# Performance work log

Hardware: AMD Instinct MI355X
Metric: run time of the kernel (lower is better)

The kernel has to match this reference:

```python
import jax, jax.numpy as jnp
import numpy as np

IN_FEATURES = 2048
OUT_FEATURES = 2048
ORDER = 8
BATCH = 8192


def setup_inputs() -> dict:
    key = jax.random.key(0)
    k1, k2, k3, k4 = jax.random.split(key, 4)
    x = jax.random.normal(k1, (BATCH, IN_FEATURES), dtype=jnp.float32)
    v = jax.random.normal(k2, (ORDER, max(IN_FEATURES, OUT_FEATURES)), dtype=jnp.float32)
    d = jax.random.normal(k3, (min(IN_FEATURES, OUT_FEATURES),), dtype=jnp.float32)
    bias = jax.random.normal(k4, (OUT_FEATURES,), dtype=jnp.float32) * 0.01
    return {"x": x, "v": v, "d": d, "bias": bias}


def reference(x, v, d, bias):
    # Normalize each reflection vector (row-wise L2 norm), as in the torch module.
    n = v.shape[1]  # max_feature = 2048
    vn = v / jnp.linalg.norm(v, axis=1, keepdims=True)
    # Householder matrices H_i = I - 2 v_i v_i^T, shape [order, n, n]
    H = jnp.eye(n, dtype=x.dtype)[None, :, :] - 2.0 * jnp.einsum('ab,ac->abc', vn, vn)
    # Chain multiply u = H_0 @ H_1 @ ... @ H_{order-1} (order is a small static constant)
    u = H[0]
    for i in range(1, H.shape[0]):
        u = u @ H[i]
    # out_features <= in_features branch: W = u @ (eye(in, out) @ diag(d))
    # eye(in, out) @ diag(d) places d on the leading diagonal of an [in, out] matrix,
    # so W = u[:, :out] * d (column scaling) -- same math, no dense diag matmul.
    W = u[:, :OUT_FEATURES] * d[None, :]
    y = x @ W + bias[None, :]
    return y
```

## Files before the change

kernel.cpp:

```cpp
#include <hip/hip_runtime.h>

#define N_FEAT 2048
#define ORDER 8
#define BATCH 8192
#define BLOCK 256
#define ROWS 4
#define NPAIR 28
#define NVAL 32

typedef float v4f __attribute__((ext_vector_type(4)));

__device__ __forceinline__ float dot4(v4f a, v4f b) {
    return a.x * b.x + a.y * b.y + a.z * b.z + a.w * b.w;
}

__global__ __launch_bounds__(BLOCK) void prep_kernel(
    const float* __restrict__ v, float* __restrict__ vn,
    float* __restrict__ Tm) {
    const int tid = threadIdx.x;
    const int lane = tid & 63, wid = tid >> 6;

    v4f a0[ORDER], a1[ORDER];
    #pragma unroll
    for (int i = 0; i < ORDER; ++i) {
        a0[i] = *(const v4f*)(v + (size_t)i * N_FEAT + tid * 4);
        a1[i] = *(const v4f*)(v + (size_t)i * N_FEAT + 1024 + tid * 4);
    }
    float ss[ORDER];
    #pragma unroll
    for (int i = 0; i < ORDER; ++i)
        ss[i] = dot4(a0[i], a0[i]) + dot4(a1[i], a1[i]);
    #pragma unroll
    for (int o = 32; o > 0; o >>= 1)
        #pragma unroll
        for (int i = 0; i < ORDER; ++i) ss[i] += __shfl_down(ss[i], o, 64);

    __shared__ float red[4][ORDER];
    __shared__ float gred[4][NPAIR];
    if (lane == 0) {
        #pragma unroll
        for (int i = 0; i < ORDER; ++i) red[wid][i] = ss[i];
    }
    __syncthreads();
    #pragma unroll
    for (int i = 0; i < ORDER; ++i) {
        const float inv = 1.0f / sqrtf(red[0][i] + red[1][i] + red[2][i] + red[3][i]);
        a0[i] *= inv; a1[i] *= inv;
        *(v4f*)(vn + (size_t)i * N_FEAT + tid * 4) = a0[i];
        *(v4f*)(vn + (size_t)i * N_FEAT + 1024 + tid * 4) = a1[i];
    }

    float gp[NPAIR];
    {
        int idx = 0;
        #pragma unroll
        for (int j = 0; j < ORDER; ++j)
            #pragma unroll
            for (int k = j + 1; k < ORDER; ++k)
                gp[idx++] = dot4(a0[j], a0[k]) + dot4(a1[j], a1[k]);
    }
    #pragma unroll
    for (int o = 32; o > 0; o >>= 1)
        #pragma unroll
        for (int q = 0; q < NPAIR; ++q) gp[q] += __shfl_down(gp[q], o, 64);
    if (lane == 0) {
        #pragma unroll
        for (int q = 0; q < NPAIR; ++q) gred[wid][q] = gp[q];
    }
    __syncthreads();

    if (tid == 0) {
        float G[ORDER][ORDER];
        {
            int idx = 0;
            #pragma unroll
            for (int j = 0; j < ORDER; ++j)
                #pragma unroll
                for (int k = j + 1; k < ORDER; ++k) {
                    G[j][k] = gred[0][idx] + gred[1][idx] + gred[2][idx] + gred[3][idx];
                    ++idx;
                }
        }
        float T[ORDER][ORDER];
        #pragma unroll
        for (int j = 0; j < ORDER; ++j)
            #pragma unroll
            for (int k = 0; k < ORDER; ++k) T[j][k] = 0.0f;
        T[0][0] = 2.0f;
        #pragma unroll
        for (int k = 1; k < ORDER; ++k) {
            #pragma unroll
            for (int j = 0; j < k; ++j) {
                float s = 0.0f;
                #pragma unroll
                for (int m = j; m < k; ++m) s += T[j][m] * G[m][k];
                T[j][k] = -2.0f * s;
            }
            T[k][k] = 2.0f;
        }
        #pragma unroll
        for (int j = 0; j < ORDER; ++j)
            #pragma unroll
            for (int k = 0; k < ORDER; ++k)
                Tm[j * ORDER + k] = T[j][k];
    }
}

__global__ __launch_bounds__(BLOCK, 3) void orth_apply_kernel(
    const float* __restrict__ x, const float* __restrict__ vn,
    const float* __restrict__ Tm, const float* __restrict__ d,
    const float* __restrict__ bias, float* __restrict__ y) {
    const int tid = threadIdx.x;
    const int lane = tid & 63;
    const size_t base = (size_t)blockIdx.x * ROWS * N_FEAT;
    const int c0 = tid * 4;
    const int c1 = 1024 + tid * 4;

    __shared__ v4f S4[NVAL / 4];
    float* Sf = (float*)S4;
    if (tid < NVAL) Sf[tid] = 0.0f;
    __syncthreads();

    v4f a0[ORDER], a1[ORDER];
    #pragma unroll
    for (int i = 0; i < ORDER; ++i) {
        a0[i] = *(const v4f*)(vn + (size_t)i * N_FEAT + c0);
        a1[i] = *(const v4f*)(vn + (size_t)i * N_FEAT + c1);
    }

    v4f z0[ROWS], z1[ROWS];
    #pragma unroll
    for (int r = 0; r < ROWS; ++r) {
        z0[r] = __builtin_nontemporal_load((const v4f*)(x + base + (size_t)r * N_FEAT + c0));
        z1[r] = __builtin_nontemporal_load((const v4f*)(x + base + (size_t)r * N_FEAT + c1));
    }

    float s[NVAL];
    #pragma unroll
    for (int i = 0; i < ORDER; ++i)
        #pragma unroll
        for (int r = 0; r < ROWS; ++r)
            s[r * ORDER + i] = dot4(z0[r], a0[i]) + dot4(z1[r], a1[i]);

    #pragma unroll
    for (int step = 0; step < 5; ++step) {
        const int m = 1 << step;
        const int n = NVAL >> step;
        #pragma unroll
        for (int j = 0; j < n / 2; ++j) {
            const float a = s[2 * j], b = s[2 * j + 1];
            const float keep = (lane & m) ? b : a;
            const float send = (lane & m) ? a : b;
            s[j] = keep + __shfl_xor(send, m, 64);
        }
    }

    atomicAdd(&Sf[lane & (NVAL - 1)], s[0]);
    __syncthreads();

    v4f Sv[NVAL / 4];
    #pragma unroll
    for (int k = 0; k < NVAL / 4; ++k) Sv[k] = S4[k];
    #define PVAL(r, j) (Sv[((r) * ORDER + (j)) >> 2][((r) * ORDER + (j)) & 3])

    float c[ROWS][ORDER];
    #pragma unroll
    for (int i = 0; i < ORDER; ++i)
        #pragma unroll
        for (int r = 0; r < ROWS; ++r) {
            float acc = 0.0f;
            #pragma unroll
            for (int j = 0; j <= i; ++j)
                acc += PVAL(r, j) * Tm[j * ORDER + i];
            c[r][i] = acc;
        }

    #pragma unroll
    for (int i = 0; i < ORDER; ++i)
        #pragma unroll
        for (int r = 0; r < ROWS; ++r) {
            z0[r] -= c[r][i] * a0[i];
            z1[r] -= c[r][i] * a1[i];
        }

    const v4f d0 = *(const v4f*)(d + c0);
    const v4f d1 = *(const v4f*)(d + c1);
    const v4f b0 = *(const v4f*)(bias + c0);
    const v4f b1 = *(const v4f*)(bias + c1);
    #pragma unroll
    for (int r = 0; r < ROWS; ++r) {
        v4f o0 = z0[r] * d0 + b0;
        v4f o1 = z1[r] * d1 + b1;
        __builtin_nontemporal_store(o0, (v4f*)(y + base + (size_t)r * N_FEAT + c0));
        __builtin_nontemporal_store(o1, (v4f*)(y + base + (size_t)r * N_FEAT + c1));
    }
}

extern "C" void kernel_launch(void* const* d_in, const int* in_sizes, int n_in,
                              void* d_out, int out_size, void* d_ws, size_t ws_size,
                              hipStream_t stream) {
    const float* x    = (const float*)d_in[0];
    const float* v    = (const float*)d_in[1];
    const float* d    = (const float*)d_in[2];
    const float* bias = (const float*)d_in[3];
    float* y  = (float*)d_out;
    float* vn = (float*)d_ws;
    float* Tm = vn + ORDER * N_FEAT;

    prep_kernel<<<1, BLOCK, 0, stream>>>(v, vn, Tm);
    orth_apply_kernel<<<BATCH / ROWS, BLOCK, 0, stream>>>(x, vn, Tm, d, bias, y);
}
```

Measured before the change: 136.8 us.

## Split fused orthogonal apply into projection and finish kernels

Splits the fused kernel into a projection kernel that writes per-row Householder coefficients to a workspace buffer and a finish kernel that rereads x and applies the correction, bias and scaling. This removes the block-wide reduction barrier from the pass that holds x in registers and allows higher occupancy in the finish pass. The cost is a second full read of x plus an extra launch. A fallback keeps the fused kernel when the workspace is too small.

```diff
diff --git a/kernel.cpp b/kernel.cpp
--- a/kernel.cpp
+++ b/kernel.cpp
@@ -103,6 +103,114 @@
             #pragma unroll
             for (int k = 0; k < ORDER; ++k)
                 Tm[j * ORDER + k] = T[j][k];
+    }
+}
+
+__global__ __launch_bounds__(BLOCK, 3) void proj_kernel(
+    const float* __restrict__ x, const float* __restrict__ vn,
+    const float* __restrict__ Tm, float* __restrict__ cbuf) {
+    const int tid = threadIdx.x;
+    const int lane = tid & 63;
+    const size_t base = (size_t)blockIdx.x * ROWS * N_FEAT;
+    const int c0 = tid * 4;
+    const int c1 = 1024 + tid * 4;
+
+    __shared__ float Sf[NVAL];
+    if (tid < NVAL) Sf[tid] = 0.0f;
+    __syncthreads();
+
+    v4f a0[ORDER], a1[ORDER];
+    #pragma unroll
+    for (int i = 0; i < ORDER; ++i) {
+        a0[i] = *(const v4f*)(vn + (size_t)i * N_FEAT + c0);
+        a1[i] = *(const v4f*)(vn + (size_t)i * N_FEAT + c1);
+    }
+    v4f z0[ROWS], z1[ROWS];
+    #pragma unroll
+    for (int r = 0; r < ROWS; ++r) {
+        z0[r] = *(const v4f*)(x + base + (size_t)r * N_FEAT + c0);
+        z1[r] = *(const v4f*)(x + base + (size_t)r * N_FEAT + c1);
+    }
+
+    float s[NVAL];
+    #pragma unroll
+    for (int i = 0; i < ORDER; ++i)
+        #pragma unroll
+        for (int r = 0; r < ROWS; ++r)
+            s[r * ORDER + i] = dot4(z0[r], a0[i]) + dot4(z1[r], a1[i]);
+
+    #pragma unroll
+    for (int step = 0; step < 5; ++step) {
+        const int m = 1 << step;
+        const int n = NVAL >> step;
+        #pragma unroll
+        for (int j = 0; j < n / 2; ++j) {
+            const float a = s[2 * j], b = s[2 * j + 1];
+            const float keep = (lane & m) ? b : a;
+            const float send = (lane & m) ? a : b;
+            s[j] = keep + __shfl_xor(send, m, 64);
+        }
+    }
+    atomicAdd(&Sf[lane & (NVAL - 1)], s[0]);
+    __syncthreads();
+
+    if (tid < NVAL) {
+        const int r = tid >> 3, i = tid & 7;
+        float acc = 0.0f;
+        #pragma unroll
+        for (int j = 0; j < ORDER; ++j)
+            if (j <= i) acc += Sf[r * ORDER + j] * Tm[j * ORDER + i];
+        cbuf[((size_t)blockIdx.x * ROWS + r) * ORDER + i] = acc;
+    }
+}
+
+__global__ __launch_bounds__(BLOCK, 4) void finish_kernel(
+    const float* __restrict__ x, const float* __restrict__ vn,
+    const float* __restrict__ cbuf, const float* __restrict__ d,
+    const float* __restrict__ bias, float* __restrict__ y) {
+    const int tid = threadIdx.x;
+    const size_t base = (size_t)blockIdx.x * ROWS * N_FEAT;
+    const int c0 = tid * 4;
+    const int c1 = 1024 + tid * 4;
+
+    v4f x0[ROWS], x1[ROWS];
+    #pragma unroll
+    for (int r = 0; r < ROWS; ++r) {
+        x0[r] = __builtin_nontemporal_load((const v4f*)(x + base + (size_t)r * N_FEAT + c0));
+        x1[r] = __builtin_nontemporal_load((const v4f*)(x + base + (size_t)r * N_FEAT + c1));
+    }
+
+    float c[ROWS][ORDER];
+    #pragma unroll
+    for (int r = 0; r < ROWS; ++r)
+        #pragma unroll
+        for (int i = 0; i < ORDER; ++i)
+            c[r][i] = cbuf[((size_t)blockIdx.x * ROWS + r) * ORDER + i];
+
+    v4f acc0[ROWS], acc1[ROWS];
+    #pragma unroll
+    for (int r = 0; r < ROWS; ++r) { acc0[r] = (v4f)0.0f; acc1[r] = (v4f)0.0f; }
+    #pragma unroll
+    for (int i = 0; i < ORDER; ++i) {
+        const v4f a0 = *(const v4f*)(vn + (size_t)i * N_FEAT + c0);
+        const v4f a1 = *(const v4f*)(vn + (size_t)i * N_FEAT + c1);
+        #pragma unroll
+        for (int r = 0; r < ROWS; ++r) {
+            acc0[r] += c[r][i] * a0;
+            acc1[r] += c[r][i] * a1;
+        }
+    }
+
+    const v4f d0 = *(const v4f*)(d + c0);
+    const v4f d1 = *(const v4f*)(d + c1);
+    const v4f b0 = *(const v4f*)(bias + c0);
+    const v4f b1 = *(const v4f*)(bias + c1);
+    #pragma unroll
+    for (int r = 0; r < ROWS; ++r) {
+        v4f o0 = (x0[r] - acc0[r]) * d0 + b0;
+        v4f o1 = (x1[r] - acc1[r]) * d1 + b1;
+        __builtin_nontemporal_store(o0, (v4f*)(y + base + (size_t)r * N_FEAT + c0));
+        __builtin_nontemporal_store(o1, (v4f*)(y + base + (size_t)r * N_FEAT + c1));
     }
 }
 
@@ -116,8 +224,7 @@
     const int c0 = tid * 4;
     const int c1 = 1024 + tid * 4;
 
-    __shared__ v4f S4[NVAL / 4];
-    float* Sf = (float*)S4;
+    __shared__ float Sf[NVAL];
     if (tid < NVAL) Sf[tid] = 0.0f;
     __syncthreads();
 
@@ -127,7 +234,6 @@
         a0[i] = *(const v4f*)(vn + (size_t)i * N_FEAT + c0);
         a1[i] = *(const v4f*)(vn + (size_t)i * N_FEAT + c1);
     }
-
     v4f z0[ROWS], z1[ROWS];
     #pragma unroll
     for (int r = 0; r < ROWS; ++r) {
@@ -154,14 +260,8 @@
             s[j] = keep + __shfl_xor(send, m, 64);
         }
     }
-
     atomicAdd(&Sf[lane & (NVAL - 1)], s[0]);
     __syncthreads();
-
-    v4f Sv[NVAL / 4];
-    #pragma unroll
-    for (int k = 0; k < NVAL / 4; ++k) Sv[k] = S4[k];
-    #define PVAL(r, j) (Sv[((r) * ORDER + (j)) >> 2][((r) * ORDER + (j)) & 3])
 
     float c[ROWS][ORDER];
     #pragma unroll
@@ -171,7 +271,7 @@
             float acc = 0.0f;
             #pragma unroll
             for (int j = 0; j <= i; ++j)
-                acc += PVAL(r, j) * Tm[j * ORDER + i];
+                acc += Sf[r * ORDER + j] * Tm[j * ORDER + i];
             c[r][i] = acc;
         }
 
@@ -206,7 +306,16 @@
     float* y  = (float*)d_out;
     float* vn = (float*)d_ws;
     float* Tm = vn + ORDER * N_FEAT;
+    float* cbuf = Tm + ORDER * ORDER;
+
+    const size_t need =
+        (size_t)(ORDER * N_FEAT + ORDER * ORDER + BATCH * ORDER) * sizeof(float);
 
     prep_kernel<<<1, BLOCK, 0, stream>>>(v, vn, Tm);
-    orth_apply_kernel<<<BATCH / ROWS, BLOCK, 0, stream>>>(x, vn, Tm, d, bias, y);
-}
+    if (ws_size >= need) {
+        proj_kernel<<<BATCH / ROWS, BLOCK, 0, stream>>>(x, vn, Tm, cbuf);
+        finish_kernel<<<BATCH / ROWS, BLOCK, 0, stream>>>(x, vn, cbuf, d, bias, y);
+    } else {
+        orth_apply_kernel<<<BATCH / ROWS, BLOCK, 0, stream>>>(x, vn, Tm, d, bias, y);
+    }
+}
```

New measurement: 136.1 us. No clear change (-0.6%).

## Use persistent blocks with software-prefetched row groups and per-wave shared reduction

Applied to the files above, without the earlier changes.

The apply kernel now launches 512 persistent blocks, each looping over four 4-row groups. The next group's x tile is loaded while the current group is reduced and written. The shared-memory atomicAdd reduction is replaced by per-wave slots in a double-buffered array, summed after a barrier, which also drops the zero-init barrier. vn, T, d and bias are loaded once per block instead of once per group. The cost is higher register pressure from holding two x tiles plus the 8x8 T matrix, and the occupancy hint in the launch bounds is removed.

```diff
diff --git a/kernel.cpp b/kernel.cpp
--- a/kernel.cpp
+++ b/kernel.cpp
@@ -7,6 +7,8 @@
 #define ROWS 4
 #define NPAIR 28
 #define NVAL 32
+#define NBLOCK 512
+#define GROUPS (BATCH / ROWS / NBLOCK)
 
 typedef float v4f __attribute__((ext_vector_type(4)));
 
@@ -106,20 +108,16 @@
     }
 }
 
-__global__ __launch_bounds__(BLOCK, 3) void orth_apply_kernel(
+__global__ __launch_bounds__(BLOCK) void orth_apply_kernel(
     const float* __restrict__ x, const float* __restrict__ vn,
     const float* __restrict__ Tm, const float* __restrict__ d,
     const float* __restrict__ bias, float* __restrict__ y) {
     const int tid = threadIdx.x;
-    const int lane = tid & 63;
-    const size_t base = (size_t)blockIdx.x * ROWS * N_FEAT;
+    const int lane = tid & 63, wid = tid >> 6;
     const int c0 = tid * 4;
     const int c1 = 1024 + tid * 4;
 
-    __shared__ v4f S4[NVAL / 4];
-    float* Sf = (float*)S4;
-    if (tid < NVAL) Sf[tid] = 0.0f;
-    __syncthreads();
+    __shared__ float Sf[2][4][NVAL];
 
     v4f a0[ORDER], a1[ORDER];
     #pragma unroll
@@ -127,72 +125,101 @@
         a0[i] = *(const v4f*)(vn + (size_t)i * N_FEAT + c0);
         a1[i] = *(const v4f*)(vn + (size_t)i * N_FEAT + c1);
     }
-
-    v4f z0[ROWS], z1[ROWS];
+    const v4f dv0 = *(const v4f*)(d + c0);
+    const v4f dv1 = *(const v4f*)(d + c1);
+    const v4f bv0 = *(const v4f*)(bias + c0);
+    const v4f bv1 = *(const v4f*)(bias + c1);
+    float Tu[ORDER][ORDER];
+    #pragma unroll
+    for (int j = 0; j < ORDER; ++j)
+        #pragma unroll
+        for (int i = j; i < ORDER; ++i)
+            Tu[j][i] = Tm[j * ORDER + i];
+
+    size_t base = (size_t)blockIdx.x * ROWS * N_FEAT;
+    v4f zc0[ROWS], zc1[ROWS];
     #pragma unroll
     for (int r = 0; r < ROWS; ++r) {
-        z0[r] = __builtin_nontemporal_load((const v4f*)(x + base + (size_t)r * N_FEAT + c0));
-        z1[r] = __builtin_nontemporal_load((const v4f*)(x + base + (size_t)r * N_FEAT + c1));
-    }
-
-    float s[NVAL];
-    #pragma unroll
-    for (int i = 0; i < ORDER; ++i)
-        #pragma unroll
-        for (int r = 0; r < ROWS; ++r)
-            s[r * ORDER + i] = dot4(z0[r], a0[i]) + dot4(z1[r], a1[i]);
-
-    #pragma unroll
-    for (int step = 0; step < 5; ++step) {
-        const int m = 1 << step;
-        const int n = NVAL >> step;
-        #pragma unroll
-        for (int j = 0; j < n / 2; ++j) {
-            const float a = s[2 * j], b = s[2 * j + 1];
-            const float keep = (lane & m) ? b : a;
-            const float send = (lane & m) ? a : b;
-            s[j] = keep + __shfl_xor(send, m, 64);
-        }
-    }
-
-    atomicAdd(&Sf[lane & (NVAL - 1)], s[0]);
-    __syncthreads();
-
-    v4f Sv[NVAL / 4];
-    #pragma unroll
-    for (int k = 0; k < NVAL / 4; ++k) Sv[k] = S4[k];
-    #define PVAL(r, j) (Sv[((r) * ORDER + (j)) >> 2][((r) * ORDER + (j)) & 3])
-
-    float c[ROWS][ORDER];
-    #pragma unroll
-    for (int i = 0; i < ORDER; ++i)
+        zc0[r] = __builtin_nontemporal_load((const v4f*)(x + base + (size_t)r * N_FEAT + c0));
+        zc1[r] = __builtin_nontemporal_load((const v4f*)(x + base + (size_t)r * N_FEAT + c1));
+    }
+
+    #pragma unroll
+    for (int t = 0; t < GROUPS; ++t) {
+        const size_t nbase =
+            (size_t)(blockIdx.x + (size_t)(t + 1) * NBLOCK) * ROWS * N_FEAT;
+        v4f zn0[ROWS], zn1[ROWS];
+        if (t + 1 < GROUPS) {
+            #pragma unroll
+            for (int r = 0; r < ROWS; ++r) {
+                zn0[r] = __builtin_nontemporal_load((const v4f*)(x + nbase + (size_t)r * N_FEAT + c0));
+                zn1[r] = __builtin_nontemporal_load((const v4f*)(x + nbase + (size_t)r * N_FEAT + c1));
+            }
+        }
+
+        float s[NVAL];
+        #pragma unroll
+        for (int i = 0; i < ORDER; ++i)
+            #pragma unroll
+            for (int r = 0; r < ROWS; ++r)
+                s[r * ORDER + i] = dot4(zc0[r], a0[i]) + dot4(zc1[r], a1[i]);
+
+        #pragma unroll
+        for (int step = 0; step < 5; ++step) {
+            const int m = 1 << step;
+            const int n = NVAL >> step;
+            #pragma unroll
+            for (int j = 0; j < n / 2; ++j) {
+                const float a = s[2 * j], b = s[2 * j + 1];
+                const float keep = (lane & m) ? b : a;
+                const float send = (lane & m) ? a : b;
+                s[j] = keep + __shfl_xor(send, m, 64);
+            }
+        }
+        const float full = s[0] + __shfl_xor(s[0], 32, 64);
+
+        const int buf = t & 1;
+        if (lane < 32) Sf[buf][wid][lane] = full;
+        __syncthreads();
+
+        const v4f* S4 = (const v4f*)&Sf[buf][0][0];
+        v4f P[NVAL / 4];
+        #pragma unroll
+        for (int k = 0; k < NVAL / 4; ++k)
+            P[k] = (S4[0 * 8 + k] + S4[1 * 8 + k]) + (S4[2 * 8 + k] + S4[3 * 8 + k]);
+        #define PV(r, j) (P[((r) * ORDER + (j)) >> 2][((r) * ORDER + (j)) & 3])
+
+        float c[ROWS][ORDER];
+        #pragma unroll
+        for (int i = 0; i < ORDER; ++i)
+            #pragma unroll
+            for (int r = 0; r < ROWS; ++r) {
+                float acc = 0.0f;
+                #pragma unroll
+                for (int j = 0; j <= i; ++j)
+                    acc += PV(r, j) * Tu[j][i];
+                c[r][i] = acc;
+            }
+
         #pragma unroll
         for (int r = 0; r < ROWS; ++r) {
-            float acc = 0.0f;
-            #pragma unroll
-            for (int j = 0; j <= i; ++j)
-                acc += PVAL(r, j) * Tm[j * ORDER + i];
-            c[r][i] = acc;
-        }
-
-    #pragma unroll
-    for (int i = 0; i < ORDER; ++i)
-        #pragma unroll
-        for (int r = 0; r < ROWS; ++r) {
-            z0[r] -= c[r][i] * a0[i];
-            z1[r] -= c[r][i] * a1[i];
-        }
-
-    const v4f d0 = *(const v4f*)(d + c0);
-    const v4f d1 = *(const v4f*)(d + c1);
-    const v4f b0 = *(const v4f*)(bias + c0);
-    const v4f b1 = *(const v4f*)(bias + c1);
-    #pragma unroll
-    for (int r = 0; r < ROWS; ++r) {
-        v4f o0 = z0[r] * d0 + b0;
-        v4f o1 = z1[r] * d1 + b1;
-        __builtin_nontemporal_store(o0, (v4f*)(y + base + (size_t)r * N_FEAT + c0));
-        __builtin_nontemporal_store(o1, (v4f*)(y + base + (size_t)r * N_FEAT + c1));
+            v4f o0 = zc0[r], o1 = zc1[r];
+            #pragma unroll
+            for (int i = 0; i < ORDER; ++i) {
+                o0 -= c[r][i] * a0[i];
+                o1 -= c[r][i] * a1[i];
+            }
+            o0 = o0 * dv0 + bv0;
+            o1 = o1 * dv1 + bv1;
+            __builtin_nontemporal_store(o0, (v4f*)(y + base + (size_t)r * N_FEAT + c0));
+            __builtin_nontemporal_store(o1, (v4f*)(y + base + (size_t)r * N_FEAT + c1));
+        }
+
+        if (t + 1 < GROUPS) {
+            base = nbase;
+            #pragma unroll
+            for (int r = 0; r < ROWS; ++r) { zc0[r] = zn0[r]; zc1[r] = zn1[r]; }
+        }
     }
 }
 
@@ -208,5 +235,5 @@
     float* Tm = vn + ORDER * N_FEAT;
 
     prep_kernel<<<1, BLOCK, 0, stream>>>(v, vn, Tm);
-    orth_apply_kernel<<<BATCH / ROWS, BLOCK, 0, stream>>>(x, vn, Tm, d, bias, y);
-}
+    orth_apply_kernel<<<NBLOCK, BLOCK, 0, stream>>>(x, vn, Tm, d, bias, y);
+}
```

After: 132.9 us. -2.8%, faster.
